# Kernel tuning notes

Measured on AMD Instinct MI355X. Metric: run time of the kernel, lower is better.

Reference implementation:

```python
import jax, jax.numpy as jnp
import numpy as np

B, L, H, D = 2, 2048, 12, 64
POLY_Q = 2.0        # from normalizer='poly_2'
NEWTON_ITERS = 6
EPS = 1e-8


def setup_inputs() -> dict:
    key = jax.random.key(0)
    kq, kk, kv = jax.random.split(key, 3)
    query = jax.random.normal(kq, (B, L, H, D), dtype=jnp.float32)
    key_t = jax.random.normal(kk, (B, L, H, D), dtype=jnp.float32)
    value = jax.random.normal(kv, (B, L, H, D), dtype=jnp.float32)
    return {"query": query, "key": key_t, "value": value}


def poly_norm(x, q=POLY_Q):
    """Replace softmax by solving sum_k 1/(-x-c)^q = 1 for c via Newton, then
    weights = 1/(-x-c)^q. x: [..., kv_len]; reductions over last axis."""
    def poly(c):
        return 1.0 / ((-x - c) ** q)
    # c0 = min(-x) - 1  ==  -max(x) - 1, guarantees (-x - c) > 0
    c = -jnp.max(x, axis=-1, keepdims=True) - 1.0
    for _ in range(NEWTON_ITERS):
        ps = jnp.sum(poly(c), axis=-1, keepdims=True)
        psd = q * jnp.sum(1.0 / ((-x - c) ** (q + 1.0)), axis=-1, keepdims=True)
        c = c - (ps - 1.0) / (psd + EPS)
    return poly(c)


def reference(query, key, value):
    depth = query.shape[-1]
    q = query / jnp.sqrt(jnp.asarray(depth, dtype=query.dtype))
    # scores: [B, H, Q, K]
    attn = jnp.einsum('bqhd,bkhd->bhqk', q, key)
    attn = poly_norm(attn, POLY_Q).astype(query.dtype)
    # out: [B, Q, H, D]
    return jnp.einsum('bhqk,bkhd->bqhd', attn, value)
```

## Files before the change

kernel.cpp:

```cpp
#include <hip/hip_runtime.h>
#include <hip/hip_bf16.h>

#define NB 2
#define NL 2048
#define NH 12
#define ND 64
#define NEWTON 6
#define WV 8
#define TPW 16

typedef __bf16 bf16x8 __attribute__((ext_vector_type(8)));
typedef float f32x4 __attribute__((ext_vector_type(4)));
typedef float f32x2 __attribute__((ext_vector_type(2)));

#define ROR_ADD(v, n)                                                         \
  (v) += __int_as_float(__builtin_amdgcn_update_dpp(                          \
      0, __float_as_int(v), 0x120 + (n), 0xF, 0xF, true))
#define ROR_MAX(v, n)                                                         \
  (v) = fmaxf((v), __int_as_float(__builtin_amdgcn_update_dpp(                \
                  0, __float_as_int(v), 0x120 + (n), 0xF, 0xF, true)))

__global__ __launch_bounds__(256) void prep(
    const float* __restrict__ kg, const float* __restrict__ vg,
    __bf16* __restrict__ kp, __bf16* __restrict__ vp) {
  __shared__ __align__(16) float kv[16][260];
  const int blk = blockIdx.x;
  const int isV = blk >= NB * 128 * 3;
  const int bk = isV ? blk - NB * 128 * 3 : blk;
  const int hg = bk % 3;
  const int kt = (bk / 3) & 127;
  const int b = bk / 384;
  const int t = threadIdx.x;
  const int w = t >> 6;
  const int lane = t & 63;
  const int quad = lane >> 4;
  const int l16 = lane & 15;

  const float* __restrict__ src = isV ? vg : kg;
#pragma unroll
  for (int i = 0; i < 4; ++i) {
    const int f = i * 1024 + t * 4;
    const int key = f >> 8;
    const int rem = f & 255;
    const size_t s =
        (size_t)(b * NL + kt * 16 + key) * (NH * ND) + hg * 256 + rem;
    *(f32x4*)(&kv[key][rem]) = *(const f32x4*)(src + s);
  }
  __syncthreads();

  const int h = hg * 4 + w;

  if (!isV) {
    const float* p = &kv[l16][w * 64 + quad * 8];
    f32x4 a0 = *(const f32x4*)(p);
    f32x4 a1 = *(const f32x4*)(p + 4);
    f32x4 a2 = *(const f32x4*)(p + 32);
    f32x4 a3 = *(const f32x4*)(p + 36);
    bf16x8 h0, h1;
#pragma unroll
    for (int j = 0; j < 4; ++j) {
      h0[j] = (__bf16)a0[j];
      h0[4 + j] = (__bf16)a1[j];
      h1[j] = (__bf16)a2[j];
      h1[4 + j] = (__bf16)a3[j];
    }
    const size_t basek =
        ((size_t)((b * NH + h) * 128 + kt) * 2) * 512 + lane * 8;
    *(bf16x8*)(kp + basek) = h0;
    *(bf16x8*)(kp + basek + 512) = h1;
  } else {
    const int halfsel = (kt >> 3) & 1;
    const int pi = (kt >> 4) * 8 + (kt & 7);
    const int q2 = quad & 1;
    const int nhalf = quad >> 1;
    const int qdst = 2 * halfsel + q2;
#pragma unroll
    for (int nn = 0; nn < 2; ++nn) {
      const int n = nhalf * 2 + nn;
      bf16x8 hv;
#pragma unroll
      for (int j = 0; j < 8; ++j)
        hv[j] = (__bf16)kv[q2 * 8 + j][w * 64 + n * 16 + l16];
      const size_t off =
          ((((size_t)(b * NH + h) * 64 + pi) * 4 + n) * 64 + qdst * 16 + l16) * 8;
      *(bf16x8*)(vp + off) = hv;
    }
  }
}

__launch_bounds__(512, 4)
__global__ void attn_poly(const float* __restrict__ qg,
                          const __bf16* __restrict__ kp,
                          const __bf16* __restrict__ vp,
                          float* __restrict__ outg) {
  __shared__ __align__(16) union ShMem {
    __bf16 wslab[16][1024];
    float ex[WV][16][68];
  } sh;
  __shared__ float redmax[WV][17];
  __shared__ float redn[NEWTON][16][2];

  const int tid = threadIdx.x;
  const int w = tid >> 6;
  const int lane = tid & 63;
  const int quad = lane >> 4;
  const int l16 = lane & 15;

  const int blk = blockIdx.x;
  const int xcd = blk & 7;
  const int slot = blk >> 3;
  const int bh = xcd * 3 + (slot >> 7);
  const int qt = slot & 127;
  const int h = bh % NH;
  const int b = bh / NH;
  const int qbase = qt * 16;

  bf16x8 q0, q1;
  {
    const float* qp = qg + ((b * NL + qbase + l16) * NH + h) * ND + quad * 8;
    f32x4 a0 = *(const f32x4*)(qp);
    f32x4 a1 = *(const f32x4*)(qp + 4);
    f32x4 a2 = *(const f32x4*)(qp + 32);
    f32x4 a3 = *(const f32x4*)(qp + 36);
#pragma unroll
    for (int j = 0; j < 4; ++j) {
      q0[j] = (__bf16)(a0[j] * 0.125f);
      q0[4 + j] = (__bf16)(a1[j] * 0.125f);
      q1[j] = (__bf16)(a2[j] * 0.125f);
      q1[4 + j] = (__bf16)(a3[j] * 0.125f);
    }
  }

  f32x2 y[TPW][2];
  {
    const __bf16* kb = kp + (size_t)bh * 131072;
#pragma unroll
    for (int t = 0; t < TPW; ++t) {
      const int ktile = w + WV * t;
      const size_t o = (size_t)ktile * 1024 + lane * 8;
      bf16x8 k0 = *(const bf16x8*)(kb + o);
      bf16x8 k1 = *(const bf16x8*)(kb + o + 512);
      f32x4 acc = {0.f, 0.f, 0.f, 0.f};
      acc = __builtin_amdgcn_mfma_f32_16x16x32_bf16(q0, k0, acc, 0, 0, 0);
      acc = __builtin_amdgcn_mfma_f32_16x16x32_bf16(q1, k1, acc, 0, 0, 0);
      y[t][0] = __builtin_shufflevector(acc, acc, 0, 1);
      y[t][1] = __builtin_shufflevector(acc, acc, 2, 3);
    }
  }

  {
    f32x2 mx2[2] = {y[0][0], y[0][1]};
#pragma unroll
    for (int t = 1; t < TPW; ++t) {
#pragma unroll
      for (int j = 0; j < 2; ++j) {
        mx2[j].x = fmaxf(mx2[j].x, y[t][j].x);
        mx2[j].y = fmaxf(mx2[j].y, y[t][j].y);
      }
    }
#pragma unroll
    for (int j = 0; j < 2; ++j) {
      ROR_MAX(mx2[j].x, 8); ROR_MAX(mx2[j].x, 4); ROR_MAX(mx2[j].x, 2); ROR_MAX(mx2[j].x, 1);
      ROR_MAX(mx2[j].y, 8); ROR_MAX(mx2[j].y, 4); ROR_MAX(mx2[j].y, 2); ROR_MAX(mx2[j].y, 1);
    }
    if (l16 < 4) {
      float v = (l16 == 0) ? mx2[0].x : (l16 == 1) ? mx2[0].y
              : (l16 == 2) ? mx2[1].x : mx2[1].y;
      redmax[w][quad * 4 + l16] = v;
    }
    if (tid < NEWTON * 16 * 2) ((float*)redn)[tid] = 0.f;
    __syncthreads();
    f32x2 negc[2];
#pragma unroll
    for (int r = 0; r < 4; ++r) {
      float m = redmax[l16 & 7][quad * 4 + r];
      ROR_MAX(m, 4); ROR_MAX(m, 2); ROR_MAX(m, 1);
      ((float*)negc)[r] = m + 1.0f;
    }
#pragma unroll
    for (int t = 0; t < TPW; ++t) {
      y[t][0] = negc[0] - y[t][0];
      y[t][1] = negc[1] - y[t][1];
    }
  }

  for (int it = 0; it < NEWTON; ++it) {
    f32x2 ps2[2] = {{0.f, 0.f}, {0.f, 0.f}};
    f32x2 psd2[2] = {{0.f, 0.f}, {0.f, 0.f}};
#pragma unroll
    for (int t = 0; t < TPW; ++t) {
#pragma unroll
      for (int j = 0; j < 2; ++j) {
        f32x2 v = y[t][j];
        float z = __builtin_amdgcn_rcpf(v.x * v.y);
        f32x2 r1 = z * __builtin_shufflevector(v, v, 1, 0);
        f32x2 r2;
        asm("v_pk_mul_f32 %0, %1, %1" : "=v"(r2) : "v"(r1));
        asm("v_pk_add_f32 %0, %0, %1" : "+v"(ps2[j]) : "v"(r2));
        asm("v_pk_fma_f32 %0, %1, %2, %0" : "+v"(psd2[j]) : "v"(r2), "v"(r1));
      }
    }
#pragma unroll
    for (int j = 0; j < 2; ++j) {
      ROR_ADD(ps2[j].x, 8);  ROR_ADD(ps2[j].x, 4);  ROR_ADD(ps2[j].x, 2);  ROR_ADD(ps2[j].x, 1);
      ROR_ADD(ps2[j].y, 8);  ROR_ADD(ps2[j].y, 4);  ROR_ADD(ps2[j].y, 2);  ROR_ADD(ps2[j].y, 1);
      ROR_ADD(psd2[j].x, 8); ROR_ADD(psd2[j].x, 4); ROR_ADD(psd2[j].x, 2); ROR_ADD(psd2[j].x, 1);
      ROR_ADD(psd2[j].y, 8); ROR_ADD(psd2[j].y, 4); ROR_ADD(psd2[j].y, 2); ROR_ADD(psd2[j].y, 1);
    }
    if (l16 < 4) {
      float a = (l16 == 0) ? ps2[0].x : (l16 == 1) ? ps2[0].y
              : (l16 == 2) ? ps2[1].x : ps2[1].y;
      float d = (l16 == 0) ? psd2[0].x : (l16 == 1) ? psd2[0].y
              : (l16 == 2) ? psd2[1].x : psd2[1].y;
      atomicAdd(&redn[it][quad * 4 + l16][0], a);
      atomicAdd(&redn[it][quad * 4 + l16][1], d);
    }
    __syncthreads();
    f32x2 dd[2];
#pragma unroll
    for (int r = 0; r < 4; ++r) {
      const f32x2 v = *(const f32x2*)(&redn[it][quad * 4 + r][0]);
      ((float*)dd)[r] =
          (v.x - 1.0f) * __builtin_amdgcn_rcpf(2.0f * v.y + 1e-8f);
    }
#pragma unroll
    for (int t = 0; t < TPW; ++t) {
      y[t][0] += dd[0];
      y[t][1] += dd[1];
    }
  }

  f32x4 oacc[4];
#pragma unroll
  for (int n = 0; n < 4; ++n) oacc[n] = (f32x4){0.f, 0.f, 0.f, 0.f};
  const __bf16* vpb = vp + (size_t)bh * 131072;
  char* slab = (char*)&sh.wslab[0][0];

#pragma unroll
  for (int hh = 0; hh < 2; ++hh) {
    if (hh) __syncthreads();

#pragma unroll
    for (int tt = 0; tt < 8; ++tt) {
      const int t = hh * 8 + tt;
      f32x2 a = y[t][0];
      f32x2 bb = y[t][1];
      float za = __builtin_amdgcn_rcpf(a.x * a.y);
      float zb = __builtin_amdgcn_rcpf(bb.x * bb.y);
      f32x2 ra = za * __builtin_shufflevector(a, a, 1, 0);
      f32x2 rb = zb * __builtin_shufflevector(bb, bb, 1, 0);
      f32x2 wa = ra * ra;
      f32x2 wb = rb * rb;
      const int c2 = ((w + WV * t) * 16 + l16) * 2 - hh * 2048;
#pragma unroll
      for (int j = 0; j < 4; ++j) {
        const int r = quad * 4 + j;
        const float wv = (j == 0) ? wa.x : (j == 1) ? wa.y
                       : (j == 2) ? wb.x : wb.y;
        *(__bf16*)(slab + r * 2048 + (c2 ^ ((r & 7) << 4))) = (__bf16)wv;
      }
    }
    __syncthreads();

#pragma unroll
    for (int pp = 0; pp < 4; ++pp) {
      const int p = hh * 4 + pp;
      const size_t vo = ((size_t)(p * 8 + w) * 4) * 512 + lane * 8;
      bf16x8 v0 = *(const bf16x8*)(vpb + vo);
      bf16x8 v1 = *(const bf16x8*)(vpb + vo + 512);
      bf16x8 v2 = *(const bf16x8*)(vpb + vo + 1024);
      bf16x8 v3 = *(const bf16x8*)(vpb + vo + 1536);

      const int c2 =
          ((16 * p + 8 * (quad >> 1) + w) * 16 + (quad & 1) * 8) * 2 - hh * 2048;
      bf16x8 aw =
          *(const bf16x8*)(slab + l16 * 2048 + (c2 ^ ((l16 & 7) << 4)));

      oacc[0] = __builtin_amdgcn_mfma_f32_16x16x32_bf16(aw, v0, oacc[0], 0, 0, 0);
      oacc[1] = __builtin_amdgcn_mfma_f32_16x16x32_bf16(aw, v1, oacc[1], 0, 0, 0);
      oacc[2] = __builtin_amdgcn_mfma_f32_16x16x32_bf16(aw, v2, oacc[2], 0, 0, 0);
      oacc[3] = __builtin_amdgcn_mfma_f32_16x16x32_bf16(aw, v3, oacc[3], 0, 0, 0);
    }
  }

  __syncthreads();
#pragma unroll
  for (int n = 0; n < 4; ++n)
#pragma unroll
    for (int r = 0; r < 4; ++r)
      sh.ex[w][quad * 4 + r][n * 16 + l16] = oacc[n][r];
  __syncthreads();
  {
    const int row = 2 * w + (lane >> 5);
    const int d = lane & 31;
    float v0 = 0.f, v1 = 0.f;
#pragma unroll
    for (int i = 0; i < WV; ++i) {
      v0 += sh.ex[i][row][d];
      v1 += sh.ex[i][row][d + 32];
    }
    const int off = ((b * NL + qbase + row) * NH + h) * ND + d;
    outg[off] = v0;
    outg[off + 32] = v1;
  }
}

extern "C" void kernel_launch(void* const* d_in, const int* in_sizes, int n_in,
                              void* d_out, int out_size, void* d_ws, size_t ws_size,
                              hipStream_t stream) {
  const float* q = (const float*)d_in[0];
  const float* k = (const float*)d_in[1];
  const float* v = (const float*)d_in[2];

  const size_t plane = (size_t)NB * NH * ND * NL;
  __bf16* kp = (__bf16*)d_ws;
  __bf16* vp = kp + plane;

  prep<<<NB * 128 * 3 * 2, 256, 0, stream>>>(k, v, kp, vp);

  attn_poly<<<NB * NH * (NL / 16), 512, 0, stream>>>(
      q, kp, vp, (float*)d_out);
}
```

Before: 217.0 us.

## Replace block-shared weight slab with per-wave double-buffered LDS tiles

Each wave now writes its own normalized bf16 weight tiles into a private double-buffered LDS region and consumes them directly in the PV MFMA loop. This removes the block-wide weight slab and the __syncthreads barriers between the weight-write and MFMA phases. Weight generation for the next step is interleaved with the current MFMA step. It relies on a manual s_waitcnt for intra-wave ordering and changes which keys each wave contracts, so correctness depends on the per-wave tile layout matching the V packing.

```diff
diff --git a/kernel.cpp b/kernel.cpp
--- a/kernel.cpp
+++ b/kernel.cpp
@@ -93,10 +93,13 @@
                           const __bf16* __restrict__ kp,
                           const __bf16* __restrict__ vp,
                           float* __restrict__ outg) {
-  __shared__ __align__(16) union ShMem {
-    __bf16 wslab[16][1024];
-    float ex[WV][16][68];
-  } sh;
+  struct PW {
+    union {
+      float ex[16][68];
+      __bf16 ws[2][16][40];
+    };
+  };
+  __shared__ __align__(16) PW pw[WV];
   __shared__ float redmax[WV][17];
   __shared__ float redn[NEWTON][16][2];
 
@@ -234,61 +237,64 @@
 #pragma unroll
   for (int n = 0; n < 4; ++n) oacc[n] = (f32x4){0.f, 0.f, 0.f, 0.f};
   const __bf16* vpb = vp + (size_t)bh * 131072;
-  char* slab = (char*)&sh.wslab[0][0];
-
-#pragma unroll
-  for (int hh = 0; hh < 2; ++hh) {
-    if (hh) __syncthreads();
-
-#pragma unroll
-    for (int tt = 0; tt < 8; ++tt) {
-      const int t = hh * 8 + tt;
-      f32x2 a = y[t][0];
-      f32x2 bb = y[t][1];
-      float za = __builtin_amdgcn_rcpf(a.x * a.y);
-      float zb = __builtin_amdgcn_rcpf(bb.x * bb.y);
-      f32x2 ra = za * __builtin_shufflevector(a, a, 1, 0);
-      f32x2 rb = zb * __builtin_shufflevector(bb, bb, 1, 0);
-      f32x2 wa = ra * ra;
-      f32x2 wb = rb * rb;
-      const int c2 = ((w + WV * t) * 16 + l16) * 2 - hh * 2048;
-#pragma unroll
-      for (int j = 0; j < 4; ++j) {
-        const int r = quad * 4 + j;
-        const float wv = (j == 0) ? wa.x : (j == 1) ? wa.y
-                       : (j == 2) ? wb.x : wb.y;
-        *(__bf16*)(slab + r * 2048 + (c2 ^ ((r & 7) << 4))) = (__bf16)wv;
+
+#pragma unroll
+  for (int ts = 0; ts < 2; ++ts) {
+    f32x2 a = y[ts][0];
+    f32x2 bb = y[ts][1];
+    float za = __builtin_amdgcn_rcpf(a.x * a.y);
+    float zb = __builtin_amdgcn_rcpf(bb.x * bb.y);
+    f32x2 ra = za * __builtin_shufflevector(a, a, 1, 0);
+    f32x2 rb = zb * __builtin_shufflevector(bb, bb, 1, 0);
+    f32x2 wa = ra * ra;
+    f32x2 wb = rb * rb;
+    pw[w].ws[0][quad * 4 + 0][ts * 16 + l16] = (__bf16)wa.x;
+    pw[w].ws[0][quad * 4 + 1][ts * 16 + l16] = (__bf16)wa.y;
+    pw[w].ws[0][quad * 4 + 2][ts * 16 + l16] = (__bf16)wb.x;
+    pw[w].ws[0][quad * 4 + 3][ts * 16 + l16] = (__bf16)wb.y;
+  }
+
+#pragma unroll
+  for (int p = 0; p < 8; ++p) {
+    const size_t vo = ((size_t)(p * 8 + w) * 4) * 512 + lane * 8;
+    bf16x8 v0 = *(const bf16x8*)(vpb + vo);
+    bf16x8 v1 = *(const bf16x8*)(vpb + vo + 512);
+    bf16x8 v2 = *(const bf16x8*)(vpb + vo + 1024);
+    bf16x8 v3 = *(const bf16x8*)(vpb + vo + 1536);
+
+    asm volatile("s_waitcnt lgkmcnt(0)" ::: "memory");
+    bf16x8 aw = *(const bf16x8*)(&pw[w].ws[p & 1][l16][quad * 8]);
+
+    if (p < 7) {
+#pragma unroll
+      for (int ts = 0; ts < 2; ++ts) {
+        const int t = 2 * (p + 1) + ts;
+        f32x2 a = y[t][0];
+        f32x2 bb = y[t][1];
+        float za = __builtin_amdgcn_rcpf(a.x * a.y);
+        float zb = __builtin_amdgcn_rcpf(bb.x * bb.y);
+        f32x2 ra = za * __builtin_shufflevector(a, a, 1, 0);
+        f32x2 rb = zb * __builtin_shufflevector(bb, bb, 1, 0);
+        f32x2 wa = ra * ra;
+        f32x2 wb = rb * rb;
+        pw[w].ws[(p + 1) & 1][quad * 4 + 0][ts * 16 + l16] = (__bf16)wa.x;
+        pw[w].ws[(p + 1) & 1][quad * 4 + 1][ts * 16 + l16] = (__bf16)wa.y;
+        pw[w].ws[(p + 1) & 1][quad * 4 + 2][ts * 16 + l16] = (__bf16)wb.x;
+        pw[w].ws[(p + 1) & 1][quad * 4 + 3][ts * 16 + l16] = (__bf16)wb.y;
       }
     }
-    __syncthreads();
-
-#pragma unroll
-    for (int pp = 0; pp < 4; ++pp) {
-      const int p = hh * 4 + pp;
-      const size_t vo = ((size_t)(p * 8 + w) * 4) * 512 + lane * 8;
-      bf16x8 v0 = *(const bf16x8*)(vpb + vo);
-      bf16x8 v1 = *(const bf16x8*)(vpb + vo + 512);
-      bf16x8 v2 = *(const bf16x8*)(vpb + vo + 1024);
-      bf16x8 v3 = *(const bf16x8*)(vpb + vo + 1536);
-
-      const int c2 =
-          ((16 * p + 8 * (quad >> 1) + w) * 16 + (quad & 1) * 8) * 2 - hh * 2048;
-      bf16x8 aw =
-          *(const bf16x8*)(slab + l16 * 2048 + (c2 ^ ((l16 & 7) << 4)));
-
-      oacc[0] = __builtin_amdgcn_mfma_f32_16x16x32_bf16(aw, v0, oacc[0], 0, 0, 0);
-      oacc[1] = __builtin_amdgcn_mfma_f32_16x16x32_bf16(aw, v1, oacc[1], 0, 0, 0);
-      oacc[2] = __builtin_amdgcn_mfma_f32_16x16x32_bf16(aw, v2, oacc[2], 0, 0, 0);
-      oacc[3] = __builtin_amdgcn_mfma_f32_16x16x32_bf16(aw, v3, oacc[3], 0, 0, 0);
-    }
-  }
-
-  __syncthreads();
+
+    oacc[0] = __builtin_amdgcn_mfma_f32_16x16x32_bf16(aw, v0, oacc[0], 0, 0, 0);
+    oacc[1] = __builtin_amdgcn_mfma_f32_16x16x32_bf16(aw, v1, oacc[1], 0, 0, 0);
+    oacc[2] = __builtin_amdgcn_mfma_f32_16x16x32_bf16(aw, v2, oacc[2], 0, 0, 0);
+    oacc[3] = __builtin_amdgcn_mfma_f32_16x16x32_bf16(aw, v3, oacc[3], 0, 0, 0);
+  }
+
 #pragma unroll
   for (int n = 0; n < 4; ++n)
 #pragma unroll
     for (int r = 0; r < 4; ++r)
-      sh.ex[w][quad * 4 + r][n * 16 + l16] = oacc[n][r];
+      pw[w].ex[quad * 4 + r][n * 16 + l16] = oacc[n][r];
   __syncthreads();
   {
     const int row = 2 * w + (lane >> 5);
@@ -296,8 +302,8 @@
     float v0 = 0.f, v1 = 0.f;
 #pragma unroll
     for (int i = 0; i < WV; ++i) {
-      v0 += sh.ex[i][row][d];
-      v1 += sh.ex[i][row][d + 32];
+      v0 += pw[i].ex[row][d];
+      v1 += pw[i].ex[row][d + 32];
     }
     const int off = ((b * NL + qbase + row) * NH + h) * ND + d;
     outg[off] = v0;
```

Result: faster. 211.8 us (median of 2 runs) (-2.4%).
